# Kernel tuning notes

Measured on AMD Instinct MI355X. Metric: run time of the kernel, lower is better.

The kernel has to match this reference:

```python
import jax, jax.numpy as jnp
import numpy as np

EPS = 1e-8
LN_EPS = 1e-5
DIM, NHEADS = 512, 8
HEAD_DIM = DIM // NHEADS
SCALE = HEAD_DIM ** -0.5
ROLE_VOCAB = 8


def _layernorm(x, g, b):
    mu = x.mean(-1, keepdims=True)
    var = ((x - mu) ** 2).mean(-1, keepdims=True)
    return (x - mu) * jax.lax.rsqrt(var + LN_EPS) * g + b


def setup_inputs() -> dict:
    key = jax.random.key(0)
    ks = jax.random.split(key, 16)
    B, K, L, D = 8, 4, 1024, DIM
    s = 1.0 / np.sqrt(D)
    return {
        "state_repr": jax.random.normal(ks[0], (B, K, L, D), jnp.float32),
        "residue_mask": jax.random.randint(ks[1], (B, K, L), 0, 2) > 0,
        "state_weights": jax.random.uniform(ks[2], (B, K), jnp.float32),
        "state_roles": jax.random.randint(ks[3], (B, K), 0, ROLE_VOCAB),
        "state_present_mask": jnp.ones((B, K), dtype=bool),
        "role_emb": jax.random.normal(ks[4], (ROLE_VOCAB, D), jnp.float32),
        "Wq": jax.random.normal(ks[5], (D, D), jnp.float32) * s,
        "Wk": jax.random.normal(ks[6], (D, D), jnp.float32) * s,
        "Wv": jax.random.normal(ks[7], (D, D), jnp.float32) * s,
        "Wo": jax.random.normal(ks[8], (D, D), jnp.float32) * s,
        "ln1_g": jnp.ones((3 * D,), jnp.float32),
        "ln1_b": jnp.zeros((3 * D,), jnp.float32),
        "Wg1": jax.random.normal(ks[9], (D, 3 * D), jnp.float32) / np.sqrt(3 * D),
        "bg1": jnp.zeros((D,), jnp.float32),
        "Wg2": jax.random.normal(ks[10], (D, D), jnp.float32) * s,
        "bg2": jnp.zeros((D,), jnp.float32),
        "norm_g": jnp.ones((D,), jnp.float32),
        "norm_b": jnp.zeros((D,), jnp.float32),
    }


def _forward(state_repr, residue_mask, state_weights, state_roles, state_present_mask,
             role_emb, Wq, Wk, Wv, Wo, ln1_g, ln1_b, Wg1, bg1, Wg2, bg2, norm_g, norm_b):
    B, K, L, D = state_repr.shape
    H, hd = NHEADS, HEAD_DIM
    roles = jnp.maximum(state_roles, 0)
    role_e = role_emb[roles][:, :, None, :]                       # [B,K,1,D]
    valid = residue_mask & state_present_mask[:, :, None]          # [B,K,L]

    # normalized state weights
    pres = state_present_mask.astype(jnp.float32)
    w = state_weights.astype(jnp.float32) * pres
    denom = w.sum(1, keepdims=True)
    fallback = pres / jnp.maximum(pres.sum(1, keepdims=True), 1.0)
    nsw = jnp.where(denom > EPS, w / jnp.maximum(denom, EPS), fallback)  # [B,K]

    x = (state_repr + role_e) * valid[..., None]
    x = x.transpose(0, 2, 1, 3)                                    # [B,L,K,D]
    valid_rlk = valid.transpose(0, 2, 1)                           # [B,L,K]

    def proj(W):  # torch Linear: y = x @ W.T
        return (x @ W.T).reshape(B, L, K, H, hd).transpose(0, 1, 3, 2, 4)  # [B,L,H,K,hd]

    q, k, v = proj(Wq), proj(Wk), proj(Wv)
    logits = jnp.einsum('blhqd,blhkd->blhqk', q, k) * SCALE
    logits = logits + jnp.log(jnp.maximum(nsw, EPS))[:, None, None, None, :]
    key_mask = valid_rlk[:, :, None, None, :]                      # [B,L,1,1,K]
    logits = jnp.where(key_mask, logits, -jnp.inf)
    attn = jax.nn.softmax(logits, axis=-1)
    attn = jnp.nan_to_num(attn, nan=0.0, posinf=0.0, neginf=0.0)
    attn_out = jnp.einsum('blhqk,blhkd->blhqd', attn, v)
    attn_out = attn_out.transpose(0, 1, 3, 2, 4).reshape(B, L, K, D)
    attn_out = (attn_out @ Wo.T) * valid_rlk[..., None]

    swr = nsw[:, None, :] * valid_rlk.astype(jnp.float32)          # [B,L,K]
    swr = swr / jnp.maximum(swr.sum(-1, keepdims=True), EPS)
    weighted_mean = jnp.sum(x * swr[..., None], axis=2)            # [B,L,D]
    attn_pooled = jnp.sum(attn_out * swr[..., None], axis=2)

    max_in = jnp.where(valid_rlk[..., None], x, -1e9)
    max_feat = max_in.max(axis=2)
    has_any = valid_rlk.any(axis=2, keepdims=True)
    max_feat = jnp.where(has_any, max_feat, 0.0)

    fusion_base = 0.5 * (attn_pooled + weighted_mean)
    gate_in = jnp.concatenate([attn_pooled, weighted_mean, max_feat], axis=-1)
    h = _layernorm(gate_in, ln1_g, ln1_b)
    h = jax.nn.gelu(h @ Wg1.T + bg1, approximate=False)
    gate = jax.nn.sigmoid(h @ Wg2.T + bg2)
    fused = gate * fusion_base + (1.0 - gate) * max_feat
    fused = _layernorm(fused + weighted_mean, norm_g, norm_b)

    attn_mean = attn.mean(axis=(2, 3))                             # [B,L,K]
    return fused, attn_pooled, weighted_mean, max_feat, attn_mean, nsw


def reference(state_repr, residue_mask, state_weights, state_roles, state_present_mask,
              role_emb, Wq, Wk, Wv, Wo, ln1_g, ln1_b, Wg1, bg1, Wg2, bg2, norm_g, norm_b):
    return _forward(state_repr, residue_mask, state_weights, state_roles, state_present_mask,
                    role_emb, Wq, Wk, Wv, Wo, ln1_g, ln1_b, Wg1, bg1, Wg2, bg2, norm_g, norm_b)
```

## Files before the change

kernel.cpp:

```cpp
#include <hip/hip_runtime.h>
#include <math.h>

#define BB 8
#define KK 4
#define LL 1024
#define DD 512
#define HD 64
#define D3 1536
#define MM (BB*LL*KK)
#define BL (BB*LL)
#define SCALE 0.125f
#define EPSF 1e-8f
#define LN_EPSF 1e-5f

typedef _Float16 hfrag __attribute__((ext_vector_type(8)));
typedef float f32x4 __attribute__((ext_vector_type(4)));

__device__ __forceinline__ unsigned short f2h(float f) {
    _Float16 h = (_Float16)f;
    unsigned short u; __builtin_memcpy(&u, &h, 2); return u;
}
__device__ __forceinline__ float h2f(unsigned short u) {
    _Float16 h; __builtin_memcpy(&h, &u, 2); return (float)h;
}

__device__ __forceinline__ void glds16(const unsigned short* g, unsigned short* l) {
    __builtin_amdgcn_global_load_lds(
        (const __attribute__((address_space(1))) void*)g,
        (__attribute__((address_space(3))) void*)l, 16, 0, 0);
}

__device__ __forceinline__ void nsw_compute(const float* sw, const int* pres,
                                            int b, float* nswv) {
    float w[KK], pr[KK]; float denom = 0.f, ps = 0.f;
    #pragma unroll
    for (int k = 0; k < KK; ++k) {
        pr[k] = pres[b*KK + k] ? 1.f : 0.f;
        w[k]  = sw[b*KK + k] * pr[k];
        denom += w[k]; ps += pr[k];
    }
    #pragma unroll
    for (int k = 0; k < KK; ++k)
        nswv[k] = (denom > EPSF) ? w[k] / fmaxf(denom, EPSF)
                                 : pr[k] / fmaxf(ps, 1.f);
}

#define WSZ 262144
#define OG1 1048576
#define OG2 1835008
#define WTOT 2097152
__global__ __launch_bounds__(256) void cvt_weights(
        const float* __restrict__ Wq, const float* __restrict__ Wk,
        const float* __restrict__ Wv, const float* __restrict__ Wo,
        const float* __restrict__ Wg1, const float* __restrict__ Wg2,
        unsigned short* __restrict__ dst) {
    int t = blockIdx.x * 256 + threadIdx.x;
    int e = t * 4;
    const float* src; int off;
    if      (e < WSZ)    { src = Wq;  off = e; }
    else if (e < 2*WSZ)  { src = Wk;  off = e - WSZ; }
    else if (e < 3*WSZ)  { src = Wv;  off = e - 2*WSZ; }
    else if (e < OG1)    { src = Wo;  off = e - 3*WSZ; }
    else if (e < OG2)    { src = Wg1; off = e - OG1; }
    else                 { src = Wg2; off = e - OG2; }
    float4 v = *(const float4*)(src + off);
    ushort4 o;
    o.x = f2h(v.x); o.y = f2h(v.y); o.z = f2h(v.z); o.w = f2h(v.w);
    *(ushort4*)(dst + e) = o;
}

__global__ __launch_bounds__(256) void buildx_kernel(
        const float* __restrict__ SR, const int* __restrict__ residue,
        const int* __restrict__ pres, const int* __restrict__ roles,
        const float* __restrict__ role_emb, const float* __restrict__ sw,
        unsigned short* __restrict__ Xh, float* __restrict__ rowmask,
        float* __restrict__ out_wm, float* __restrict__ out_mx,
        float* __restrict__ f_nsw) {
    int t  = blockIdx.x * 256 + threadIdx.x;
    int bl = t >> 7;
    int d4 = (t & 127) << 2;
    int b  = bl >> 10, l = bl & 1023;
    float nswv[KK];
    nsw_compute(sw, pres, b, nswv);
    float mk[KK], swr[KK];
    float ssum = 0.f, many = 0.f;
    #pragma unroll
    for (int k = 0; k < KK; ++k) {
        int bk = b*KK + k;
        bool valid = (residue[(size_t)bk*LL + l] != 0) && (pres[bk] != 0);
        mk[k]  = valid ? 1.f : 0.f;
        swr[k] = nswv[k] * mk[k];
        ssum += swr[k]; many += mk[k];
    }
    float inv = 1.f / fmaxf(ssum, EPSF);
    bool hasany = many > 0.5f;
    float wmx = 0.f, wmy = 0.f, wmz = 0.f, wmw = 0.f;
    float mxx = -1e9f, mxy = -1e9f, mxz = -1e9f, mxw = -1e9f;
    #pragma unroll
    for (int k = 0; k < KK; ++k) {
        int bk = b*KK + k;
        int role = roles[bk]; if (role < 0) role = 0;
        float4 sr = *(const float4*)(SR + ((size_t)bk*LL + l)*DD + d4);
        float4 re = *(const float4*)(role_emb + (size_t)role*DD + d4);
        float xx = (sr.x + re.x)*mk[k], xy = (sr.y + re.y)*mk[k];
        float xz = (sr.z + re.z)*mk[k], xw = (sr.w + re.w)*mk[k];
        ushort4 xs; xs.x = f2h(xx); xs.y = f2h(xy); xs.z = f2h(xz); xs.w = f2h(xw);
        *(ushort4*)(Xh + (size_t)(bl*KK + k)*DD + d4) = xs;
        float s = swr[k]*inv;
        wmx = fmaf(xx, s, wmx); wmy = fmaf(xy, s, wmy);
        wmz = fmaf(xz, s, wmz); wmw = fmaf(xw, s, wmw);
        if (mk[k] > 0.5f) {
            mxx = fmaxf(mxx, xx); mxy = fmaxf(mxy, xy);
            mxz = fmaxf(mxz, xz); mxw = fmaxf(mxw, xw);
        }
    }
    if (!hasany) { mxx = mxy = mxz = mxw = 0.f; }
    float4 wmv; wmv.x = wmx; wmv.y = wmy; wmv.z = wmz; wmv.w = wmw;
    float4 mxv; mxv.x = mxx; mxv.y = mxy; mxv.z = mxz; mxv.w = mxw;
    *(float4*)(out_wm + (size_t)bl*DD + d4) = wmv;
    *(float4*)(out_mx + (size_t)bl*DD + d4) = mxv;
    if (d4 == 0) {
        #pragma unroll
        for (int k = 0; k < KK; ++k) rowmask[bl*KK + k] = mk[k];
    }
    if (blockIdx.x == 0 && threadIdx.x < BB*KK) {
        int bb = threadIdx.x >> 2, kk2 = threadIdx.x & 3;
        float nv[KK];
        nsw_compute(sw, pres, bb, nv);
        f_nsw[threadIdx.x] = nv[kk2];
    }
}

__global__ __launch_bounds__(512, 4) void gemm_qkv_8p(
        const unsigned short* __restrict__ A, const unsigned short* __restrict__ W,
        unsigned short* __restrict__ Cbase) {
    __shared__ __align__(16) unsigned short smem[36864];
    const int tid  = threadIdx.x;
    const int wave = tid >> 6, lane = tid & 63;
    const int id = blockIdx.x;
    const int wg = (id & 7) * 192 + (id >> 3);
    const int m0 = (wg / 12) * 256;
    const int n0 = (wg % 12) * 128;
    const int wm = wave >> 1, wn = wave & 1;
    const int fr = lane & 15, q = lane >> 4;
    const int srow = tid >> 2, scc = tid & 3;
    const int sswz = (scc ^ ((srow >> 1) & 3)) << 3;
    const unsigned short* Ag0 = A + (size_t)(m0 + srow)*512 + sswz;
    const unsigned short* Ag1 = Ag0 + (size_t)128*512;
    const unsigned short* Wg0 = W + (size_t)(n0 + srow)*512 + sswz;
    const int lA0 = tid << 3;
    const int lA1 = (tid + 512) << 3;
    int aoff[4], boff[4];
    #pragma unroll
    for (int mf = 0; mf < 4; ++mf) {
        int row = (wm << 6) + (mf << 4) + fr;
        aoff[mf] = (row << 5) + ((q ^ ((row >> 1) & 3)) << 3);
    }
    #pragma unroll
    for (int nf = 0; nf < 4; ++nf) {
        int row = (wn << 6) + (nf << 4) + fr;
        boff[nf] = (row << 5) + ((q ^ ((row >> 1) & 3)) << 3);
    }
    f32x4 acc[4][4] = {};

#define VMWAIT(N) asm volatile("s_waitcnt vmcnt(" #N ")" ::: "memory")
#define STAGE(tt) do { unsigned short* _d = smem + ((tt) % 3) * 12288; \
        const int _ko = (tt) << 5; \
        glds16(Ag0 + _ko, _d + lA0); glds16(Ag1 + _ko, _d + lA1); \
        glds16(Wg0 + _ko, _d + 8192 + lA0); } while (0)
#define MFROW(ai, areg) \
        acc[ai][0] = __builtin_amdgcn_mfma_f32_16x16x32_f16(areg, b0, acc[ai][0], 0, 0, 0); \
        acc[ai][1] = __builtin_amdgcn_mfma_f32_16x16x32_f16(areg, b1, acc[ai][1], 0, 0, 0); \
        acc[ai][2] = __builtin_amdgcn_mfma_f32_16x16x32_f16(areg, b2, acc[ai][2], 0, 0, 0); \
        acc[ai][3] = __builtin_amdgcn_mfma_f32_16x16x32_f16(areg, b3, acc[ai][3], 0, 0, 0);
#define TILE(t, STG, VM) do { \
        const unsigned short* _Ab = smem + ((t) % 3) * 12288; \
        const unsigned short* _Bb = _Ab + 8192; \
        VMWAIT(VM); \
        __builtin_amdgcn_s_barrier(); \
        __builtin_amdgcn_sched_barrier(0); \
        hfrag b0 = *(const hfrag*)(_Bb + boff[0]); \
        hfrag b1 = *(const hfrag*)(_Bb + boff[1]); \
        hfrag b2 = *(const hfrag*)(_Bb + boff[2]); \
        hfrag b3 = *(const hfrag*)(_Bb + boff[3]); \
        hfrag a0_ = *(const hfrag*)(_Ab + aoff[0]); \
        hfrag a1_ = *(const hfrag*)(_Ab + aoff[1]); \
        hfrag a2_ = *(const hfrag*)(_Ab + aoff[2]); \
        hfrag a3_ = *(const hfrag*)(_Ab + aoff[3]); \
        if (STG) STAGE((t) + 2); \
        __builtin_amdgcn_s_setprio(1); \
        MFROW(0, a0_) MFROW(1, a1_) MFROW(2, a2_) MFROW(3, a3_) \
        __builtin_amdgcn_s_setprio(0); \
    } while (0)

    STAGE(0); STAGE(1);
    #pragma unroll
    for (int t = 0; t < 14; ++t) TILE(t, 1, 3);
    TILE(14, 0, 3);
    TILE(15, 0, 0);
#undef TILE
#undef MFROW
#undef STAGE
#undef VMWAIT

    const int gc0 = n0 + (wn << 6);
    const int seg = gc0 >> 9;
    unsigned short* Cs = Cbase + (size_t)seg * ((size_t)MM * 512);
    const int cb = gc0 & 511;
    #pragma unroll
    for (int mf = 0; mf < 4; ++mf) {
        const int grow = m0 + (wm << 6) + (mf << 4) + (q << 2);
        #pragma unroll
        for (int nf = 0; nf < 4; ++nf) {
            const int col = cb + (nf << 4) + fr;
            #pragma unroll
            for (int r = 0; r < 4; ++r)
                Cs[(size_t)(grow + r) * 512 + col] = f2h(acc[mf][nf][r]);
        }
    }
}

__global__ __launch_bounds__(512, 4) void wo_gemm(
        const unsigned short* __restrict__ A,
        const unsigned short* __restrict__ W,
        const float* __restrict__ sw, const int* __restrict__ pres,
        const float* __restrict__ rmask, float* __restrict__ out_ap) {
    __shared__ __align__(16) unsigned short smem[36864];
    const int tid  = threadIdx.x;
    const int wave = tid >> 6, lane = tid & 63;
    const int id = blockIdx.x;
    const int wg = (id & 7) * 64 + (id >> 3);
    const int m0 = (wg >> 2) * 256;
    const int n0 = (wg & 3) * 128;
    const int wm = wave >> 1, wn = wave & 1;
    const int fr = lane & 15, q = lane >> 4;
    const int srow = tid >> 2, scc = tid & 3;
    const int sswz = (scc ^ ((srow >> 1) & 3)) << 3;
    const unsigned short* Ag0 = A + (size_t)(m0 + srow)*512 + sswz;
    const unsigned short* Ag1 = Ag0 + (size_t)128*512;
    const unsigned short* Wg0 = W + (size_t)(n0 + srow)*512 + sswz;
    const int lA0 = tid << 3;
    const int lA1 = (tid + 512) << 3;
    int aoff[4], boff[4];
    #pragma unroll
    for (int mf = 0; mf < 4; ++mf) {
        int row = (wm << 6) + (mf << 4) + fr;
        aoff[mf] = (row << 5) + ((q ^ ((row >> 1) & 3)) << 3);
    }
    #pragma unroll
    for (int nf = 0; nf < 4; ++nf) {
        int row = (wn << 6) + (nf << 4) + fr;
        boff[nf] = (row << 5) + ((q ^ ((row >> 1) & 3)) << 3);
    }
    f32x4 acc[4][4] = {};

#define VMWAIT(N) asm volatile("s_waitcnt vmcnt(" #N ")" ::: "memory")
#define STAGE(tt) do { unsigned short* _d = smem + ((tt) % 3) * 12288; \
        const int _ko = (tt) << 5; \
        glds16(Ag0 + _ko, _d + lA0); glds16(Ag1 + _ko, _d + lA1); \
        glds16(Wg0 + _ko, _d + 8192 + lA0); } while (0)
#define MFROW(ai, areg) \
        acc[ai][0] = __builtin_amdgcn_mfma_f32_16x16x32_f16(areg, b0, acc[ai][0], 0, 0, 0); \
        acc[ai][1] = __builtin_amdgcn_mfma_f32_16x16x32_f16(areg, b1, acc[ai][1], 0, 0, 0); \
        acc[ai][2] = __builtin_amdgcn_mfma_f32_16x16x32_f16(areg, b2, acc[ai][2], 0, 0, 0); \
        acc[ai][3] = __builtin_amdgcn_mfma_f32_16x16x32_f16(areg, b3, acc[ai][3], 0, 0, 0);
#define TILE(t, STG, VM) do { \
        const unsigned short* _Ab = smem + ((t) % 3) * 12288; \
        const unsigned short* _Bb = _Ab + 8192; \
        VMWAIT(VM); \
        __builtin_amdgcn_s_barrier(); \
        __builtin_amdgcn_sched_barrier(0); \
        hfrag b0 = *(const hfrag*)(_Bb + boff[0]); \
        hfrag b1 = *(const hfrag*)(_Bb + boff[1]); \
        hfrag b2 = *(const hfrag*)(_Bb + boff[2]); \
        hfrag b3 = *(const hfrag*)(_Bb + boff[3]); \
        hfrag a0_ = *(const hfrag*)(_Ab + aoff[0]); \
        hfrag a1_ = *(const hfrag*)(_Ab + aoff[1]); \
        hfrag a2_ = *(const hfrag*)(_Ab + aoff[2]); \
        hfrag a3_ = *(const hfrag*)(_Ab + aoff[3]); \
        if (STG) STAGE((t) + 2); \
        __builtin_amdgcn_s_setprio(1); \
        MFROW(0, a0_) MFROW(1, a1_) MFROW(2, a2_) MFROW(3, a3_) \
        __builtin_amdgcn_s_setprio(0); \
    } while (0)

    STAGE(0); STAGE(1);
    #pragma unroll
    for (int t = 0; t < 14; ++t) TILE(t, 1, 3);
    TILE(14, 0, 3);
    TILE(15, 0, 0);
#undef TILE
#undef MFROW
#undef STAGE
#undef VMWAIT

    const int b = (m0 >> 2) >> 10;
    float nv[KK];
    nsw_compute(sw, pres, b, nv);
    #pragma unroll
    for (int mf = 0; mf < 4; ++mf) {
        const int grow = m0 + (wm << 6) + (mf << 4) + (q << 2);
        const int bl = grow >> 2;
        float s4[KK]; float ssum = 0.f;
        #pragma unroll
        for (int k = 0; k < KK; ++k) { s4[k] = nv[k] * rmask[bl*4 + k]; ssum += s4[k]; }
        const float inv = 1.f / fmaxf(ssum, EPSF);
        #pragma unroll
        for (int nf = 0; nf < 4; ++nf) {
            const int col = n0 + (wn << 6) + (nf << 4) + fr;
            float ap = 0.f;
            #pragma unroll
            for (int r = 0; r < KK; ++r) ap = fmaf(s4[r]*inv, acc[mf][nf][r], ap);
            out_ap[(size_t)bl*512 + col] = ap;
        }
    }
}

__global__ __launch_bounds__(256) void ln1_kernel(
        const float* __restrict__ ap, const float* __restrict__ wm,
        const float* __restrict__ mx, const float* __restrict__ g,
        const float* __restrict__ bvec, unsigned short* __restrict__ hin) {
    const int bl = blockIdx.x * 4 + (threadIdx.x >> 6);
    const int lane = threadIdx.x & 63;
    const int c0 = lane * 8;
    float4 v[3][2];
    const float* srcs[3] = { ap + (size_t)bl*512 + c0,
                             wm + (size_t)bl*512 + c0,
                             mx + (size_t)bl*512 + c0 };
    float s = 0.f, s2 = 0.f;
    #pragma unroll
    for (int sg = 0; sg < 3; ++sg) {
        v[sg][0] = *(const float4*)(srcs[sg]);
        v[sg][1] = *(const float4*)(srcs[sg] + 4);
        #pragma unroll
        for (int e = 0; e < 8; ++e) {
            float x = ((const float*)v[sg])[e];
            s += x; s2 += x*x;
        }
    }
    #pragma unroll
    for (int o = 1; o < 64; o <<= 1) {
        s  += __shfl_xor(s,  o, 64);
        s2 += __shfl_xor(s2, o, 64);
    }
    const float mu = s * (1.f/(float)D3);
    const float var = s2 * (1.f/(float)D3) - mu*mu;
    const float rstd = rsqrtf(var + LN_EPSF);
    #pragma unroll
    for (int sg = 0; sg < 3; ++sg) {
        const int gofs = sg*512 + c0;
        #pragma unroll
        for (int h = 0; h < 2; ++h) {
            float4 g4 = *(const float4*)(g + gofs + h*4);
            float4 b4 = *(const float4*)(bvec + gofs + h*4);
            const float* sv = (const float*)&v[sg][h];
            ushort4 o4;
            o4.x = f2h((sv[0]-mu)*rstd*g4.x + b4.x);
            o4.y = f2h((sv[1]-mu)*rstd*g4.y + b4.y);
            o4.z = f2h((sv[2]-mu)*rstd*g4.z + b4.z);
            o4.w = f2h((sv[3]-mu)*rstd*g4.w + b4.w);
            *(ushort4*)(hin + (size_t)bl*D3 + gofs + h*4) = o4;
        }
    }
}

__global__ __launch_bounds__(256, 3) void gemm_g1(
        const unsigned short* __restrict__ A, const unsigned short* __restrict__ W,
        unsigned short* __restrict__ C, const float* __restrict__ bias) {
    __shared__ __align__(16) unsigned short smem[24576];
    const int tid  = threadIdx.x;
    const int wave = tid >> 6, lane = tid & 63;
    const int id = blockIdx.x;
    const int wg = (id & 7) * 32 + (id >> 3);
    const int m0 = (wg >> 2) * 128;
    const int n0 = (wg & 3) * 128;
    const int wm = wave >> 1, wn = wave & 1;
    const int fr = lane & 15, q = lane >> 4;
    const int srow = tid >> 2, scc = tid & 3;
    const int sswz = (scc ^ ((srow >> 1) & 3)) << 3;
    const unsigned short* Ag0 = A + (size_t)(m0 + srow)*D3 + sswz;
    const unsigned short* Ag1 = Ag0 + (size_t)64*D3;
    const unsigned short* Wg0 = W + (size_t)(n0 + srow)*D3 + sswz;
    const unsigned short* Wg1p = Wg0 + (size_t)64*D3;
    const int lA0 = tid << 3;
    const int lA1 = (tid + 256) << 3;
    int aoff[4], boff[4];
    #pragma unroll
    for (int mf = 0; mf < 4; ++mf) {
        int row = (wm << 6) + (mf << 4) + fr;
        aoff[mf] = (row << 5) + ((q ^ ((row >> 1) & 3)) << 3);
    }
    #pragma unroll
    for (int nf = 0; nf < 4; ++nf) {
        int row = (wn << 6) + (nf << 4) + fr;
        boff[nf] = (row << 5) + ((q ^ ((row >> 1) & 3)) << 3);
    }
    f32x4 acc[4][4] = {};

#define VMWAIT(N) asm volatile("s_waitcnt vmcnt(" #N ")" ::: "memory")
#define STAGE(tt) do { unsigned short* _d = smem + ((tt) % 3) * 8192; \
        const int _ko = (tt) << 5; \
        glds16(Ag0 + _ko, _d + lA0); glds16(Ag1 + _ko, _d + lA1); \
        glds16(Wg0 + _ko, _d + 4096 + lA0); glds16(Wg1p + _ko, _d + 4096 + lA1); } while (0)
#define MFROW(ai, areg) \
        acc[ai][0] = __builtin_amdgcn_mfma_f32_16x16x32_f16(areg, b0, acc[ai][0], 0, 0, 0); \
        acc[ai][1] = __builtin_amdgcn_mfma_f32_16x16x32_f16(areg, b1, acc[ai][1], 0, 0, 0); \
        acc[ai][2] = __builtin_amdgcn_mfma_f32_16x16x32_f16(areg, b2, acc[ai][2], 0, 0, 0); \
        acc[ai][3] = __builtin_amdgcn_mfma_f32_16x16x32_f16(areg, b3, acc[ai][3], 0, 0, 0);
#define TILE(t, STG, VM) do { \
        const unsigned short* _Ab = smem + ((t) % 3) * 8192; \
        const unsigned short* _Bb = _Ab + 4096; \
        VMWAIT(VM); \
        __builtin_amdgcn_s_barrier(); \
        __builtin_amdgcn_sched_barrier(0); \
        hfrag b0 = *(const hfrag*)(_Bb + boff[0]); \
        hfrag b1 = *(const hfrag*)(_Bb + boff[1]); \
        hfrag b2 = *(const hfrag*)(_Bb + boff[2]); \
        hfrag b3 = *(const hfrag*)(_Bb + boff[3]); \
        hfrag a0_ = *(const hfrag*)(_Ab + aoff[0]); \
        hfrag a1_ = *(const hfrag*)(_Ab + aoff[1]); \
        hfrag a2_ = *(const hfrag*)(_Ab + aoff[2]); \
        hfrag a3_ = *(const hfrag*)(_Ab + aoff[3]); \
        if (STG) STAGE((t) + 2); \
        __builtin_amdgcn_s_setprio(1); \
        MFROW(0, a0_) MFROW(1, a1_) MFROW(2, a2_) MFROW(3, a3_) \
        __builtin_amdgcn_s_setprio(0); \
    } while (0)

    STAGE(0); STAGE(1);
    #pragma unroll 3
    for (int t = 0; t < 46; ++t) TILE(t, 1, 4);
    TILE(46, 0, 4);
    TILE(47, 0, 0);
#undef TILE
#undef MFROW
#undef STAGE
#undef VMWAIT

    #pragma unroll
    for (int mf = 0; mf < 4; ++mf) {
        const int grow = m0 + (wm << 6) + (mf << 4) + (q << 2);
        #pragma unroll
        for (int nf = 0; nf < 4; ++nf) {
            const int col = n0 + (wn << 6) + (nf << 4) + fr;
            const float bv = bias[col];
            #pragma unroll
            for (int r = 0; r < 4; ++r) {
                float v = acc[mf][nf][r] + bv;
                v = 0.5f * v * (1.f + erff(v * 0.70710678118654752f));
                C[(size_t)(grow + r) * 512 + col] = f2h(v);
            }
        }
    }
}

__global__ __launch_bounds__(256, 3) void wg2_gemm(
        const unsigned short* __restrict__ A,
        const unsigned short* __restrict__ W,
        const float* __restrict__ bg2,
        const float* __restrict__ in_ap, const float* __restrict__ in_wm,
        const float* __restrict__ in_mx, float* __restrict__ pre) {
    __shared__ __align__(16) unsigned short smem[24576];
    const int tid  = threadIdx.x;
    const int wave = tid >> 6, lane = tid & 63;
    const int id = blockIdx.x;
    const int wg = (id & 7) * 32 + (id >> 3);
    const int m0 = (wg >> 2) * 128;
    const int n0 = (wg & 3) * 128;
    const int wm = wave >> 1, wn = wave & 1;
    const int fr = lane & 15, q = lane >> 4;
    const int srow = tid >> 2, scc = tid & 3;
    const int sswz = (scc ^ ((srow >> 1) & 3)) << 3;
    const unsigned short* Ag0 = A + (size_t)(m0 + srow)*512 + sswz;
    const unsigned short* Ag1 = Ag0 + (size_t)64*512;
    const unsigned short* Wg0 = W + (size_t)(n0 + srow)*512 + sswz;
    const unsigned short* Wg1p = Wg0 + (size_t)64*512;
    const int lA0 = tid << 3;
    const int lA1 = (tid + 256) << 3;
    int aoff[4], boff[4];
    #pragma unroll
    for (int mf = 0; mf < 4; ++mf) {
        int row = (wm << 6) + (mf << 4) + fr;
        aoff[mf] = (row << 5) + ((q ^ ((row >> 1) & 3)) << 3);
    }
    #pragma unroll
    for (int nf = 0; nf < 4; ++nf) {
        int row = (wn << 6) + (nf << 4) + fr;
        boff[nf] = (row << 5) + ((q ^ ((row >> 1) & 3)) << 3);
    }
    f32x4 acc[4][4] = {};

#define VMWAIT(N) asm volatile("s_waitcnt vmcnt(" #N ")" ::: "memory")
#define STAGE(tt) do { unsigned short* _d = smem + ((tt) % 3) * 8192; \
        const int _ko = (tt) << 5; \
        glds16(Ag0 + _ko, _d + lA0); glds16(Ag1 + _ko, _d + lA1); \
        glds16(Wg0 + _ko, _d + 4096 + lA0); glds16(Wg1p + _ko, _d + 4096 + lA1); } while (0)
#define MFROW(ai, areg) \
        acc[ai][0] = __builtin_amdgcn_mfma_f32_16x16x32_f16(areg, b0, acc[ai][0], 0, 0, 0); \
        acc[ai][1] = __builtin_amdgcn_mfma_f32_16x16x32_f16(areg, b1, acc[ai][1], 0, 0, 0); \
        acc[ai][2] = __builtin_amdgcn_mfma_f32_16x16x32_f16(areg, b2, acc[ai][2], 0, 0, 0); \
        acc[ai][3] = __builtin_amdgcn_mfma_f32_16x16x32_f16(areg, b3, acc[ai][3], 0, 0, 0);
#define TILE(t, STG, VM) do { \
        const unsigned short* _Ab = smem + ((t) % 3) * 8192; \
        const unsigned short* _Bb = _Ab + 4096; \
        VMWAIT(VM); \
        __builtin_amdgcn_s_barrier(); \
        __builtin_amdgcn_sched_barrier(0); \
        hfrag b0 = *(const hfrag*)(_Bb + boff[0]); \
        hfrag b1 = *(const hfrag*)(_Bb + boff[1]); \
        hfrag b2 = *(const hfrag*)(_Bb + boff[2]); \
        hfrag b3 = *(const hfrag*)(_Bb + boff[3]); \
        hfrag a0_ = *(const hfrag*)(_Ab + aoff[0]); \
        hfrag a1_ = *(const hfrag*)(_Ab + aoff[1]); \
        hfrag a2_ = *(const hfrag*)(_Ab + aoff[2]); \
        hfrag a3_ = *(const hfrag*)(_Ab + aoff[3]); \
        if (STG) STAGE((t) + 2); \
        __builtin_amdgcn_s_setprio(1); \
        MFROW(0, a0_) MFROW(1, a1_) MFROW(2, a2_) MFROW(3, a3_) \
        __builtin_amdgcn_s_setprio(0); \
    } while (0)

    STAGE(0); STAGE(1);
    #pragma unroll
    for (int t = 0; t < 14; ++t) TILE(t, 1, 4);
    TILE(14, 0, 4);
    TILE(15, 0, 0);
#undef TILE
#undef MFROW
#undef STAGE
#undef VMWAIT

    #pragma unroll
    for (int mf = 0; mf < 4; ++mf) {
        const int grow = m0 + (wm << 6) + (mf << 4) + (q << 2);
        #pragma unroll
        for (int nf = 0; nf < 4; ++nf) {
            const int col = n0 + (wn << 6) + (nf << 4) + fr;
            const float bv = bg2[col];
            #pragma unroll
            for (int r = 0; r < 4; ++r) {
                const int row = grow + r;
                float g = 1.f / (1.f + expf(-(acc[mf][nf][r] + bv)));
                float ap = in_ap[(size_t)row*512 + col];
                float wmv = in_wm[(size_t)row*512 + col];
                float mxv = in_mx[(size_t)row*512 + col];
                pre[(size_t)row*512 + col] = g*0.5f*(ap + wmv) + (1.f - g)*mxv + wmv;
            }
        }
    }
}

__global__ __launch_bounds__(256) void final_ln_kernel(
        const float* __restrict__ pre, const float* __restrict__ ng,
        const float* __restrict__ nb, float* __restrict__ fused) {
    const int row = blockIdx.x * 4 + (threadIdx.x >> 6);
    const int lane = threadIdx.x & 63;
    const int c0 = lane * 8;
    float4 p0 = *(const float4*)(pre + (size_t)row*512 + c0);
    float4 p1 = *(const float4*)(pre + (size_t)row*512 + c0 + 4);
    float s = 0.f, s2 = 0.f;
    const float* pv = (const float*)&p0;
    #pragma unroll
    for (int e = 0; e < 4; ++e) { s += pv[e]; s2 += pv[e]*pv[e]; }
    pv = (const float*)&p1;
    #pragma unroll
    for (int e = 0; e < 4; ++e) { s += pv[e]; s2 += pv[e]*pv[e]; }
    #pragma unroll
    for (int o = 1; o < 64; o <<= 1) {
        s  += __shfl_xor(s,  o, 64);
        s2 += __shfl_xor(s2, o, 64);
    }
    const float mu = s * (1.f/(float)DD);
    const float var = s2 * (1.f/(float)DD) - mu*mu;
    const float rstd = rsqrtf(var + LN_EPSF);
    float4 g0 = *(const float4*)(ng + c0), g1 = *(const float4*)(ng + c0 + 4);
    float4 b0 = *(const float4*)(nb + c0), b1 = *(const float4*)(nb + c0 + 4);
    float4 o0, o1;
    o0.x = (p0.x-mu)*rstd*g0.x + b0.x; o0.y = (p0.y-mu)*rstd*g0.y + b0.y;
    o0.z = (p0.z-mu)*rstd*g0.z + b0.z; o0.w = (p0.w-mu)*rstd*g0.w + b0.w;
    o1.x = (p1.x-mu)*rstd*g1.x + b1.x; o1.y = (p1.y-mu)*rstd*g1.y + b1.y;
    o1.z = (p1.z-mu)*rstd*g1.z + b1.z; o1.w = (p1.w-mu)*rstd*g1.w + b1.w;
    *(float4*)(fused + (size_t)row*512 + c0) = o0;
    *(float4*)(fused + (size_t)row*512 + c0 + 4) = o1;
}

__global__ __launch_bounds__(256) void attn_kernel(
        unsigned short* Qb ,
        const unsigned short* __restrict__ Kb, const unsigned short* __restrict__ Vb,
        const float* __restrict__ sw, const int* __restrict__ pres,
        const float* __restrict__ rowmask,
        float* __restrict__ attn_mean_out) {
    __shared__ float att[128];
    __shared__ float lw[KK], mk[KK];
    int bl = blockIdx.x, b = bl >> 10, mb = bl * KK;
    int tid = threadIdx.x;
    if (tid < KK) {
        float nv[KK];
        nsw_compute(sw, pres, b, nv);
        lw[tid] = logf(fmaxf(nv[tid], EPSF));
        mk[tid] = rowmask[mb + tid];
    }
    __syncthreads();
    if (tid < 128) {
        int h = tid >> 4, i = (tid >> 2) & 3, j = tid & 3;
        const unsigned short* qp = Qb + (size_t)(mb + i)*DD + h*HD;
        const unsigned short* kp = Kb + (size_t)(mb + j)*DD + h*HD;
        float s = 0.f;
        #pragma unroll
        for (int c = 0; c < 8; ++c) {
            hfrag qv = *(const hfrag*)(qp + c*8);
            hfrag kv = *(const hfrag*)(kp + c*8);
            #pragma unroll
            for (int e = 0; e < 8; ++e)
                s = fmaf((float)qv[e], (float)kv[e], s);
        }
        float lg = s * SCALE + lw[j];
        att[tid] = (mk[j] > 0.5f) ? lg : -INFINITY;
    }
    __syncthreads();
    if (tid < 32) {
        int base = tid * 4;
        float l0 = att[base], l1 = att[base+1], l2 = att[base+2], l3 = att[base+3];
        float m = fmaxf(fmaxf(l0, l1), fmaxf(l2, l3));
        if (m == -INFINITY) {
            att[base] = att[base+1] = att[base+2] = att[base+3] = 0.f;
        } else {
            float e0 = expf(l0 - m), e1 = expf(l1 - m), e2 = expf(l2 - m), e3 = expf(l3 - m);
            float inv = 1.f / (e0 + e1 + e2 + e3);
            att[base] = e0*inv; att[base+1] = e1*inv; att[base+2] = e2*inv; att[base+3] = e3*inv;
        }
    }
    __syncthreads();
    if (tid < KK) {
        float s = 0.f;
        for (int hi = 0; hi < 32; ++hi) s += att[hi*4 + tid];
        attn_mean_out[(size_t)bl*KK + tid] = s * (1.f/32.f);
    }
    #pragma unroll
    for (int p = 0; p < 4; ++p) {
        int idx = p*256 + tid;
        int i = idx >> 8, d2 = (idx & 255) << 1, h = d2 >> 6;
        float s0 = 0.f, s1 = 0.f;
        #pragma unroll
        for (int j = 0; j < KK; ++j) {
            float aj = att[h*16 + i*4 + j];
            ushort2 vv = *(const ushort2*)(Vb + (size_t)(mb + j)*DD + d2);
            s0 = fmaf(aj, h2f(vv.x), s0);
            s1 = fmaf(aj, h2f(vv.y), s1);
        }
        ushort2 o; o.x = f2h(s0); o.y = f2h(s1);
        *(ushort2*)(Qb + (size_t)(mb + i)*DD + d2) = o;
    }
}

extern "C" void kernel_launch(void* const* d_in, const int* in_sizes, int n_in,
                              void* d_out, int out_size, void* d_ws, size_t ws_size,
                              hipStream_t stream) {
    const float* SR      = (const float*)d_in[0];
    const int*   residue = (const int*)d_in[1];
    const float* sw      = (const float*)d_in[2];
    const int*   roles   = (const int*)d_in[3];
    const int*   pres    = (const int*)d_in[4];
    const float* role_emb= (const float*)d_in[5];
    const float* Wq      = (const float*)d_in[6];
    const float* Wk      = (const float*)d_in[7];
    const float* Wv      = (const float*)d_in[8];
    const float* Wo      = (const float*)d_in[9];
    const float* ln1_g   = (const float*)d_in[10];
    const float* ln1_b   = (const float*)d_in[11];
    const float* Wg1     = (const float*)d_in[12];
    const float* bg1     = (const float*)d_in[13];
    const float* Wg2     = (const float*)d_in[14];
    const float* bg2     = (const float*)d_in[15];
    const float* norm_g  = (const float*)d_in[16];
    const float* norm_b  = (const float*)d_in[17];

    float* out = (float*)d_out;
    const size_t BLD = (size_t)BL * DD;
    float* f_fused = out;
    float* f_ap    = out + BLD;
    float* f_wm    = out + 2*BLD;
    float* f_mx    = out + 3*BLD;
    float* f_am    = out + 4*BLD;
    float* f_nsw   = out + 4*BLD + (size_t)BL*KK;

    char* base = (char*)d_ws;
    const size_t MD2 = (size_t)MM * DD * 2;
    unsigned short* Xh = (unsigned short*)(base);
    unsigned short* Qh = (unsigned short*)(base + MD2);
    unsigned short* Kh = (unsigned short*)(base + 2*MD2);
    unsigned short* Vh = (unsigned short*)(base + 3*MD2);
    unsigned short* Wb = (unsigned short*)(base + 4*MD2);
    float* rmask = (float*)(base + 4*MD2 + (size_t)WTOT*2);
    unsigned short* AOh  = Qh;
    unsigned short* Hin  = Vh;
    unsigned short* Hbuf = Xh;
    float* preb = (float*)Kh;
    const unsigned short* Wqkv = Wb;
    const unsigned short* Woh  = Wb + 3*WSZ;
    const unsigned short* Wg1h = Wb + OG1;
    const unsigned short* Wg2h = Wb + OG2;

    dim3 blk(256);

    cvt_weights<<<WTOT/1024, blk, 0, stream>>>(Wq, Wk, Wv, Wo, Wg1, Wg2, Wb);
    buildx_kernel<<<(BL*128)/256, blk, 0, stream>>>(SR, residue, pres, roles, role_emb,
                                                    sw, Xh, rmask, f_wm, f_mx, f_nsw);

    gemm_qkv_8p<<<dim3(1536), dim3(512), 0, stream>>>(Xh, Wqkv, Qh);

    attn_kernel<<<BL, blk, 0, stream>>>(Qh, Kh, Vh, sw, pres, rmask, f_am);

    wo_gemm<<<dim3(512), dim3(512), 0, stream>>>(
        AOh, Woh, sw, pres, rmask, f_ap);

    ln1_kernel<<<dim3(BL/4), blk, 0, stream>>>(
        f_ap, f_wm, f_mx, ln1_g, ln1_b, Hin);

    gemm_g1<<<dim3(256), blk, 0, stream>>>(Hin, Wg1h, Hbuf, bg1);

    wg2_gemm<<<dim3(256), blk, 0, stream>>>(
        Hbuf, Wg2h, bg2, f_ap, f_wm, f_mx, preb);

    final_ln_kernel<<<dim3(BL/4), blk, 0, stream>>>(
        preb, norm_g, norm_b, f_fused);
}
```

Before: 335.2 us.

## Pool attention outputs over states before Wo projection to shrink GEMM

Because the state-weighted pooling over K is linear, the attention kernel now folds the pooling weights into the attention probabilities and writes one pooled value vector per residue. The output projection then runs on a BL×512 matrix instead of a (BL·K)×512 one, so the Wo GEMM does a quarter of the work and no longer has to write the per-state attention output. The attention kernel also writes less data. The cost is a small extra reduction inside the attention kernel and a slightly different rounding order because fp16 rounding now happens after pooling rather than before.

```diff
diff --git a/kernel.cpp b/kernel.cpp
--- a/kernel.cpp
+++ b/kernel.cpp
@@ -220,153 +220,89 @@
     }
 }
 
-__global__ __launch_bounds__(512, 4) void wo_gemm(
+__global__ __launch_bounds__(256) void attn_kernel(
+        const unsigned short* __restrict__ Qb, const unsigned short* __restrict__ Kb,
+        const unsigned short* __restrict__ Vb,
+        unsigned short* __restrict__ pooled,
+        const float* __restrict__ sw, const int* __restrict__ pres,
+        const float* __restrict__ rowmask,
+        float* __restrict__ attn_mean_out) {
+    __shared__ float att[128];
+    __shared__ float wv[32];
+    __shared__ float lw[KK], mk[KK], sp[KK];
+    int bl = blockIdx.x, b = bl >> 10, mb = bl * KK;
+    int tid = threadIdx.x;
+    if (tid < KK) {
+        float nv[KK];
+        nsw_compute(sw, pres, b, nv);
+        lw[tid] = logf(fmaxf(nv[tid], EPSF));
+        float mkk[KK]; float ssum = 0.f;
+        #pragma unroll
+        for (int k = 0; k < KK; ++k) { mkk[k] = rowmask[mb + k]; ssum += nv[k]*mkk[k]; }
+        mk[tid] = mkk[tid];
+        sp[tid] = nv[tid]*mkk[tid] / fmaxf(ssum, EPSF);
+    }
+    __syncthreads();
+    if (tid < 128) {
+        int h = tid >> 4, i = (tid >> 2) & 3, j = tid & 3;
+        const unsigned short* qp = Qb + (size_t)(mb + i)*DD + h*HD;
+        const unsigned short* kp = Kb + (size_t)(mb + j)*DD + h*HD;
+        float s = 0.f;
+        #pragma unroll
+        for (int c = 0; c < 8; ++c) {
+            hfrag qv = *(const hfrag*)(qp + c*8);
+            hfrag kv = *(const hfrag*)(kp + c*8);
+            #pragma unroll
+            for (int e = 0; e < 8; ++e)
+                s = fmaf((float)qv[e], (float)kv[e], s);
+        }
+        float lg = s * SCALE + lw[j];
+        att[tid] = (mk[j] > 0.5f) ? lg : -INFINITY;
+    }
+    __syncthreads();
+    if (tid < 32) {
+        int base = tid * 4;
+        float l0 = att[base], l1 = att[base+1], l2 = att[base+2], l3 = att[base+3];
+        float m = fmaxf(fmaxf(l0, l1), fmaxf(l2, l3));
+        if (m == -INFINITY) {
+            att[base] = att[base+1] = att[base+2] = att[base+3] = 0.f;
+        } else {
+            float e0 = expf(l0 - m), e1 = expf(l1 - m), e2 = expf(l2 - m), e3 = expf(l3 - m);
+            float inv = 1.f / (e0 + e1 + e2 + e3);
+            att[base] = e0*inv; att[base+1] = e1*inv; att[base+2] = e2*inv; att[base+3] = e3*inv;
+        }
+    }
+    __syncthreads();
+    if (tid < KK) {
+        float s = 0.f;
+        for (int hi = 0; hi < 32; ++hi) s += att[hi*4 + tid];
+        attn_mean_out[(size_t)bl*KK + tid] = s * (1.f/32.f);
+    }
+    if (tid < 32) {
+        int h = tid >> 2, j = tid & 3;
+        wv[tid] = sp[0]*att[h*16 + 0*4 + j] + sp[1]*att[h*16 + 1*4 + j]
+                + sp[2]*att[h*16 + 2*4 + j] + sp[3]*att[h*16 + 3*4 + j];
+    }
+    __syncthreads();
+    {
+        int d2 = tid << 1, h = d2 >> 6;
+        float s0 = 0.f, s1 = 0.f;
+        #pragma unroll
+        for (int j = 0; j < KK; ++j) {
+            float aj = wv[h*4 + j];
+            ushort2 vvv = *(const ushort2*)(Vb + (size_t)(mb + j)*DD + d2);
+            s0 = fmaf(aj, h2f(vvv.x), s0);
+            s1 = fmaf(aj, h2f(vvv.y), s1);
+        }
+        ushort2 o; o.x = f2h(s0); o.y = f2h(s1);
+        *(ushort2*)(pooled + (size_t)bl*DD + d2) = o;
+    }
+}
+
+__global__ __launch_bounds__(256, 3) void ap_gemm(
         const unsigned short* __restrict__ A,
         const unsigned short* __restrict__ W,
-        const float* __restrict__ sw, const int* __restrict__ pres,
-        const float* __restrict__ rmask, float* __restrict__ out_ap) {
-    __shared__ __align__(16) unsigned short smem[36864];
-    const int tid  = threadIdx.x;
-    const int wave = tid >> 6, lane = tid & 63;
-    const int id = blockIdx.x;
-    const int wg = (id & 7) * 64 + (id >> 3);
-    const int m0 = (wg >> 2) * 256;
-    const int n0 = (wg & 3) * 128;
-    const int wm = wave >> 1, wn = wave & 1;
-    const int fr = lane & 15, q = lane >> 4;
-    const int srow = tid >> 2, scc = tid & 3;
-    const int sswz = (scc ^ ((srow >> 1) & 3)) << 3;
-    const unsigned short* Ag0 = A + (size_t)(m0 + srow)*512 + sswz;
-    const unsigned short* Ag1 = Ag0 + (size_t)128*512;
-    const unsigned short* Wg0 = W + (size_t)(n0 + srow)*512 + sswz;
-    const int lA0 = tid << 3;
-    const int lA1 = (tid + 512) << 3;
-    int aoff[4], boff[4];
-    #pragma unroll
-    for (int mf = 0; mf < 4; ++mf) {
-        int row = (wm << 6) + (mf << 4) + fr;
-        aoff[mf] = (row << 5) + ((q ^ ((row >> 1) & 3)) << 3);
-    }
-    #pragma unroll
-    for (int nf = 0; nf < 4; ++nf) {
-        int row = (wn << 6) + (nf << 4) + fr;
-        boff[nf] = (row << 5) + ((q ^ ((row >> 1) & 3)) << 3);
-    }
-    f32x4 acc[4][4] = {};
-
-#define VMWAIT(N) asm volatile("s_waitcnt vmcnt(" #N ")" ::: "memory")
-#define STAGE(tt) do { unsigned short* _d = smem + ((tt) % 3) * 12288; \
-        const int _ko = (tt) << 5; \
-        glds16(Ag0 + _ko, _d + lA0); glds16(Ag1 + _ko, _d + lA1); \
-        glds16(Wg0 + _ko, _d + 8192 + lA0); } while (0)
-#define MFROW(ai, areg) \
-        acc[ai][0] = __builtin_amdgcn_mfma_f32_16x16x32_f16(areg, b0, acc[ai][0], 0, 0, 0); \
-        acc[ai][1] = __builtin_amdgcn_mfma_f32_16x16x32_f16(areg, b1, acc[ai][1], 0, 0, 0); \
-        acc[ai][2] = __builtin_amdgcn_mfma_f32_16x16x32_f16(areg, b2, acc[ai][2], 0, 0, 0); \
-        acc[ai][3] = __builtin_amdgcn_mfma_f32_16x16x32_f16(areg, b3, acc[ai][3], 0, 0, 0);
-#define TILE(t, STG, VM) do { \
-        const unsigned short* _Ab = smem + ((t) % 3) * 12288; \
-        const unsigned short* _Bb = _Ab + 8192; \
-        VMWAIT(VM); \
-        __builtin_amdgcn_s_barrier(); \
-        __builtin_amdgcn_sched_barrier(0); \
-        hfrag b0 = *(const hfrag*)(_Bb + boff[0]); \
-        hfrag b1 = *(const hfrag*)(_Bb + boff[1]); \
-        hfrag b2 = *(const hfrag*)(_Bb + boff[2]); \
-        hfrag b3 = *(const hfrag*)(_Bb + boff[3]); \
-        hfrag a0_ = *(const hfrag*)(_Ab + aoff[0]); \
-        hfrag a1_ = *(const hfrag*)(_Ab + aoff[1]); \
-        hfrag a2_ = *(const hfrag*)(_Ab + aoff[2]); \
-        hfrag a3_ = *(const hfrag*)(_Ab + aoff[3]); \
-        if (STG) STAGE((t) + 2); \
-        __builtin_amdgcn_s_setprio(1); \
-        MFROW(0, a0_) MFROW(1, a1_) MFROW(2, a2_) MFROW(3, a3_) \
-        __builtin_amdgcn_s_setprio(0); \
-    } while (0)
-
-    STAGE(0); STAGE(1);
-    #pragma unroll
-    for (int t = 0; t < 14; ++t) TILE(t, 1, 3);
-    TILE(14, 0, 3);
-    TILE(15, 0, 0);
-#undef TILE
-#undef MFROW
-#undef STAGE
-#undef VMWAIT
-
-    const int b = (m0 >> 2) >> 10;
-    float nv[KK];
-    nsw_compute(sw, pres, b, nv);
-    #pragma unroll
-    for (int mf = 0; mf < 4; ++mf) {
-        const int grow = m0 + (wm << 6) + (mf << 4) + (q << 2);
-        const int bl = grow >> 2;
-        float s4[KK]; float ssum = 0.f;
-        #pragma unroll
-        for (int k = 0; k < KK; ++k) { s4[k] = nv[k] * rmask[bl*4 + k]; ssum += s4[k]; }
-        const float inv = 1.f / fmaxf(ssum, EPSF);
-        #pragma unroll
-        for (int nf = 0; nf < 4; ++nf) {
-            const int col = n0 + (wn << 6) + (nf << 4) + fr;
-            float ap = 0.f;
-            #pragma unroll
-            for (int r = 0; r < KK; ++r) ap = fmaf(s4[r]*inv, acc[mf][nf][r], ap);
-            out_ap[(size_t)bl*512 + col] = ap;
-        }
-    }
-}
-
-__global__ __launch_bounds__(256) void ln1_kernel(
-        const float* __restrict__ ap, const float* __restrict__ wm,
-        const float* __restrict__ mx, const float* __restrict__ g,
-        const float* __restrict__ bvec, unsigned short* __restrict__ hin) {
-    const int bl = blockIdx.x * 4 + (threadIdx.x >> 6);
-    const int lane = threadIdx.x & 63;
-    const int c0 = lane * 8;
-    float4 v[3][2];
-    const float* srcs[3] = { ap + (size_t)bl*512 + c0,
-                             wm + (size_t)bl*512 + c0,
-                             mx + (size_t)bl*512 + c0 };
-    float s = 0.f, s2 = 0.f;
-    #pragma unroll
-    for (int sg = 0; sg < 3; ++sg) {
-        v[sg][0] = *(const float4*)(srcs[sg]);
-        v[sg][1] = *(const float4*)(srcs[sg] + 4);
-        #pragma unroll
-        for (int e = 0; e < 8; ++e) {
-            float x = ((const float*)v[sg])[e];
-            s += x; s2 += x*x;
-        }
-    }
-    #pragma unroll
-    for (int o = 1; o < 64; o <<= 1) {
-        s  += __shfl_xor(s,  o, 64);
-        s2 += __shfl_xor(s2, o, 64);
-    }
-    const float mu = s * (1.f/(float)D3);
-    const float var = s2 * (1.f/(float)D3) - mu*mu;
-    const float rstd = rsqrtf(var + LN_EPSF);
-    #pragma unroll
-    for (int sg = 0; sg < 3; ++sg) {
-        const int gofs = sg*512 + c0;
-        #pragma unroll
-        for (int h = 0; h < 2; ++h) {
-            float4 g4 = *(const float4*)(g + gofs + h*4);
-            float4 b4 = *(const float4*)(bvec + gofs + h*4);
-            const float* sv = (const float*)&v[sg][h];
-            ushort4 o4;
-            o4.x = f2h((sv[0]-mu)*rstd*g4.x + b4.x);
-            o4.y = f2h((sv[1]-mu)*rstd*g4.y + b4.y);
-            o4.z = f2h((sv[2]-mu)*rstd*g4.z + b4.z);
-            o4.w = f2h((sv[3]-mu)*rstd*g4.w + b4.w);
-            *(ushort4*)(hin + (size_t)bl*D3 + gofs + h*4) = o4;
-        }
-    }
-}
-
-__global__ __launch_bounds__(256, 3) void gemm_g1(
-        const unsigned short* __restrict__ A, const unsigned short* __restrict__ W,
-        unsigned short* __restrict__ C, const float* __restrict__ bias) {
+        float* __restrict__ out_ap) {
     __shared__ __align__(16) unsigned short smem[24576];
     const int tid  = threadIdx.x;
     const int wave = tid >> 6, lane = tid & 63;
@@ -378,10 +314,10 @@
     const int fr = lane & 15, q = lane >> 4;
     const int srow = tid >> 2, scc = tid & 3;
     const int sswz = (scc ^ ((srow >> 1) & 3)) << 3;
-    const unsigned short* Ag0 = A + (size_t)(m0 + srow)*D3 + sswz;
-    const unsigned short* Ag1 = Ag0 + (size_t)64*D3;
-    const unsigned short* Wg0 = W + (size_t)(n0 + srow)*D3 + sswz;
-    const unsigned short* Wg1p = Wg0 + (size_t)64*D3;
+    const unsigned short* Ag0 = A + (size_t)(m0 + srow)*512 + sswz;
+    const unsigned short* Ag1 = Ag0 + (size_t)64*512;
+    const unsigned short* Wg0 = W + (size_t)(n0 + srow)*512 + sswz;
+    const unsigned short* Wg1p = Wg0 + (size_t)64*512;
     const int lA0 = tid << 3;
     const int lA1 = (tid + 256) << 3;
     int aoff[4], boff[4];
@@ -428,10 +364,10 @@
     } while (0)
 
     STAGE(0); STAGE(1);
-    #pragma unroll 3
-    for (int t = 0; t < 46; ++t) TILE(t, 1, 4);
-    TILE(46, 0, 4);
-    TILE(47, 0, 0);
+    #pragma unroll
+    for (int t = 0; t < 14; ++t) TILE(t, 1, 4);
+    TILE(14, 0, 4);
+    TILE(15, 0, 0);
 #undef TILE
 #undef MFROW
 #undef STAGE
@@ -443,23 +379,64 @@
         #pragma unroll
         for (int nf = 0; nf < 4; ++nf) {
             const int col = n0 + (wn << 6) + (nf << 4) + fr;
-            const float bv = bias[col];
             #pragma unroll
-            for (int r = 0; r < 4; ++r) {
-                float v = acc[mf][nf][r] + bv;
-                v = 0.5f * v * (1.f + erff(v * 0.70710678118654752f));
-                C[(size_t)(grow + r) * 512 + col] = f2h(v);
-            }
-        }
-    }
-}
-
-__global__ __launch_bounds__(256, 3) void wg2_gemm(
-        const unsigned short* __restrict__ A,
-        const unsigned short* __restrict__ W,
-        const float* __restrict__ bg2,
-        const float* __restrict__ in_ap, const float* __restrict__ in_wm,
-        const float* __restrict__ in_mx, float* __restrict__ pre) {
+            for (int r = 0; r < 4; ++r)
+                out_ap[(size_t)(grow + r)*512 + col] = acc[mf][nf][r];
+        }
+    }
+}
+
+__global__ __launch_bounds__(256) void ln1_kernel(
+        const float* __restrict__ ap, const float* __restrict__ wm,
+        const float* __restrict__ mx, const float* __restrict__ g,
+        const float* __restrict__ bvec, unsigned short* __restrict__ hin) {
+    const int bl = blockIdx.x * 4 + (threadIdx.x >> 6);
+    const int lane = threadIdx.x & 63;
+    const int c0 = lane * 8;
+    float4 v[3][2];
+    const float* srcs[3] = { ap + (size_t)bl*512 + c0,
+                             wm + (size_t)bl*512 + c0,
+                             mx + (size_t)bl*512 + c0 };
+    float s = 0.f, s2 = 0.f;
+    #pragma unroll
+    for (int sg = 0; sg < 3; ++sg) {
+        v[sg][0] = *(const float4*)(srcs[sg]);
+        v[sg][1] = *(const float4*)(srcs[sg] + 4);
+        #pragma unroll
+        for (int e = 0; e < 8; ++e) {
+            float x = ((const float*)v[sg])[e];
+            s += x; s2 += x*x;
+        }
+    }
+    #pragma unroll
+    for (int o = 1; o < 64; o <<= 1) {
+        s  += __shfl_xor(s,  o, 64);
+        s2 += __shfl_xor(s2, o, 64);
+    }
+    const float mu = s * (1.f/(float)D3);
+    const float var = s2 * (1.f/(float)D3) - mu*mu;
+    const float rstd = rsqrtf(var + LN_EPSF);
+    #pragma unroll
+    for (int sg = 0; sg < 3; ++sg) {
+        const int gofs = sg*512 + c0;
+        #pragma unroll
+        for (int h = 0; h < 2; ++h) {
+            float4 g4 = *(const float4*)(g + gofs + h*4);
+            float4 b4 = *(const float4*)(bvec + gofs + h*4);
+            const float* sv = (const float*)&v[sg][h];
+            ushort4 o4;
+            o4.x = f2h((sv[0]-mu)*rstd*g4.x + b4.x);
+            o4.y = f2h((sv[1]-mu)*rstd*g4.y + b4.y);
+            o4.z = f2h((sv[2]-mu)*rstd*g4.z + b4.z);
+            o4.w = f2h((sv[3]-mu)*rstd*g4.w + b4.w);
+            *(ushort4*)(hin + (size_t)bl*D3 + gofs + h*4) = o4;
+        }
+    }
+}
+
+__global__ __launch_bounds__(256, 3) void gemm_g1(
+        const unsigned short* __restrict__ A, const unsigned short* __restrict__ W,
+        unsigned short* __restrict__ C, const float* __restrict__ bias) {
     __shared__ __align__(16) unsigned short smem[24576];
     const int tid  = threadIdx.x;
     const int wave = tid >> 6, lane = tid & 63;
@@ -471,10 +448,10 @@
     const int fr = lane & 15, q = lane >> 4;
     const int srow = tid >> 2, scc = tid & 3;
     const int sswz = (scc ^ ((srow >> 1) & 3)) << 3;
-    const unsigned short* Ag0 = A + (size_t)(m0 + srow)*512 + sswz;
-    const unsigned short* Ag1 = Ag0 + (size_t)64*512;
-    const unsigned short* Wg0 = W + (size_t)(n0 + srow)*512 + sswz;
-    const unsigned short* Wg1p = Wg0 + (size_t)64*512;
+    const unsigned short* Ag0 = A + (size_t)(m0 + srow)*D3 + sswz;
+    const unsigned short* Ag1 = Ag0 + (size_t)64*D3;
+    const unsigned short* Wg0 = W + (size_t)(n0 + srow)*D3 + sswz;
+    const unsigned short* Wg1p = Wg0 + (size_t)64*D3;
     const int lA0 = tid << 3;
     const int lA1 = (tid + 256) << 3;
     int aoff[4], boff[4];
@@ -521,6 +498,99 @@
     } while (0)
 
     STAGE(0); STAGE(1);
+    #pragma unroll 3
+    for (int t = 0; t < 46; ++t) TILE(t, 1, 4);
+    TILE(46, 0, 4);
+    TILE(47, 0, 0);
+#undef TILE
+#undef MFROW
+#undef STAGE
+#undef VMWAIT
+
+    #pragma unroll
+    for (int mf = 0; mf < 4; ++mf) {
+        const int grow = m0 + (wm << 6) + (mf << 4) + (q << 2);
+        #pragma unroll
+        for (int nf = 0; nf < 4; ++nf) {
+            const int col = n0 + (wn << 6) + (nf << 4) + fr;
+            const float bv = bias[col];
+            #pragma unroll
+            for (int r = 0; r < 4; ++r) {
+                float v = acc[mf][nf][r] + bv;
+                v = 0.5f * v * (1.f + erff(v * 0.70710678118654752f));
+                C[(size_t)(grow + r) * 512 + col] = f2h(v);
+            }
+        }
+    }
+}
+
+__global__ __launch_bounds__(256, 3) void wg2_gemm(
+        const unsigned short* __restrict__ A,
+        const unsigned short* __restrict__ W,
+        const float* __restrict__ bg2,
+        const float* __restrict__ in_ap, const float* __restrict__ in_wm,
+        const float* __restrict__ in_mx, float* __restrict__ pre) {
+    __shared__ __align__(16) unsigned short smem[24576];
+    const int tid  = threadIdx.x;
+    const int wave = tid >> 6, lane = tid & 63;
+    const int id = blockIdx.x;
+    const int wg = (id & 7) * 32 + (id >> 3);
+    const int m0 = (wg >> 2) * 128;
+    const int n0 = (wg & 3) * 128;
+    const int wm = wave >> 1, wn = wave & 1;
+    const int fr = lane & 15, q = lane >> 4;
+    const int srow = tid >> 2, scc = tid & 3;
+    const int sswz = (scc ^ ((srow >> 1) & 3)) << 3;
+    const unsigned short* Ag0 = A + (size_t)(m0 + srow)*512 + sswz;
+    const unsigned short* Ag1 = Ag0 + (size_t)64*512;
+    const unsigned short* Wg0 = W + (size_t)(n0 + srow)*512 + sswz;
+    const unsigned short* Wg1p = Wg0 + (size_t)64*512;
+    const int lA0 = tid << 3;
+    const int lA1 = (tid + 256) << 3;
+    int aoff[4], boff[4];
+    #pragma unroll
+    for (int mf = 0; mf < 4; ++mf) {
+        int row = (wm << 6) + (mf << 4) + fr;
+        aoff[mf] = (row << 5) + ((q ^ ((row >> 1) & 3)) << 3);
+    }
+    #pragma unroll
+    for (int nf = 0; nf < 4; ++nf) {
+        int row = (wn << 6) + (nf << 4) + fr;
+        boff[nf] = (row << 5) + ((q ^ ((row >> 1) & 3)) << 3);
+    }
+    f32x4 acc[4][4] = {};
+
+#define VMWAIT(N) asm volatile("s_waitcnt vmcnt(" #N ")" ::: "memory")
+#define STAGE(tt) do { unsigned short* _d = smem + ((tt) % 3) * 8192; \
+        const int _ko = (tt) << 5; \
+        glds16(Ag0 + _ko, _d + lA0); glds16(Ag1 + _ko, _d + lA1); \
+        glds16(Wg0 + _ko, _d + 4096 + lA0); glds16(Wg1p + _ko, _d + 4096 + lA1); } while (0)
+#define MFROW(ai, areg) \
+        acc[ai][0] = __builtin_amdgcn_mfma_f32_16x16x32_f16(areg, b0, acc[ai][0], 0, 0, 0); \
+        acc[ai][1] = __builtin_amdgcn_mfma_f32_16x16x32_f16(areg, b1, acc[ai][1], 0, 0, 0); \
+        acc[ai][2] = __builtin_amdgcn_mfma_f32_16x16x32_f16(areg, b2, acc[ai][2], 0, 0, 0); \
+        acc[ai][3] = __builtin_amdgcn_mfma_f32_16x16x32_f16(areg, b3, acc[ai][3], 0, 0, 0);
+#define TILE(t, STG, VM) do { \
+        const unsigned short* _Ab = smem + ((t) % 3) * 8192; \
+        const unsigned short* _Bb = _Ab + 4096; \
+        VMWAIT(VM); \
+        __builtin_amdgcn_s_barrier(); \
+        __builtin_amdgcn_sched_barrier(0); \
+        hfrag b0 = *(const hfrag*)(_Bb + boff[0]); \
+        hfrag b1 = *(const hfrag*)(_Bb + boff[1]); \
+        hfrag b2 = *(const hfrag*)(_Bb + boff[2]); \
+        hfrag b3 = *(const hfrag*)(_Bb + boff[3]); \
+        hfrag a0_ = *(const hfrag*)(_Ab + aoff[0]); \
+        hfrag a1_ = *(const hfrag*)(_Ab + aoff[1]); \
+        hfrag a2_ = *(const hfrag*)(_Ab + aoff[2]); \
+        hfrag a3_ = *(const hfrag*)(_Ab + aoff[3]); \
+        if (STG) STAGE((t) + 2); \
+        __builtin_amdgcn_s_setprio(1); \
+        MFROW(0, a0_) MFROW(1, a1_) MFROW(2, a2_) MFROW(3, a3_) \
+        __builtin_amdgcn_s_setprio(0); \
+    } while (0)
+
+    STAGE(0); STAGE(1);
     #pragma unroll
     for (int t = 0; t < 14; ++t) TILE(t, 1, 4);
     TILE(14, 0, 4);
@@ -582,75 +652,6 @@
     o1.z = (p1.z-mu)*rstd*g1.z + b1.z; o1.w = (p1.w-mu)*rstd*g1.w + b1.w;
     *(float4*)(fused + (size_t)row*512 + c0) = o0;
     *(float4*)(fused + (size_t)row*512 + c0 + 4) = o1;
-}
-
-__global__ __launch_bounds__(256) void attn_kernel(
-        unsigned short* Qb ,
-        const unsigned short* __restrict__ Kb, const unsigned short* __restrict__ Vb,
-        const float* __restrict__ sw, const int* __restrict__ pres,
-        const float* __restrict__ rowmask,
-        float* __restrict__ attn_mean_out) {
-    __shared__ float att[128];
-    __shared__ float lw[KK], mk[KK];
-    int bl = blockIdx.x, b = bl >> 10, mb = bl * KK;
-    int tid = threadIdx.x;
-    if (tid < KK) {
-        float nv[KK];
-        nsw_compute(sw, pres, b, nv);
-        lw[tid] = logf(fmaxf(nv[tid], EPSF));
-        mk[tid] = rowmask[mb + tid];
-    }
-    __syncthreads();
-    if (tid < 128) {
-        int h = tid >> 4, i = (tid >> 2) & 3, j = tid & 3;
-        const unsigned short* qp = Qb + (size_t)(mb + i)*DD + h*HD;
-        const unsigned short* kp = Kb + (size_t)(mb + j)*DD + h*HD;
-        float s = 0.f;
-        #pragma unroll
-        for (int c = 0; c < 8; ++c) {
-            hfrag qv = *(const hfrag*)(qp + c*8);
-            hfrag kv = *(const hfrag*)(kp + c*8);
-            #pragma unroll
-            for (int e = 0; e < 8; ++e)
-                s = fmaf((float)qv[e], (float)kv[e], s);
-        }
-        float lg = s * SCALE + lw[j];
-        att[tid] = (mk[j] > 0.5f) ? lg : -INFINITY;
-    }
-    __syncthreads();
-    if (tid < 32) {
-        int base = tid * 4;
-        float l0 = att[base], l1 = att[base+1], l2 = att[base+2], l3 = att[base+3];
-        float m = fmaxf(fmaxf(l0, l1), fmaxf(l2, l3));
-        if (m == -INFINITY) {
-            att[base] = att[base+1] = att[base+2] = att[base+3] = 0.f;
-        } else {
-            float e0 = expf(l0 - m), e1 = expf(l1 - m), e2 = expf(l2 - m), e3 = expf(l3 - m);
-            float inv = 1.f / (e0 + e1 + e2 + e3);
-            att[base] = e0*inv; att[base+1] = e1*inv; att[base+2] = e2*inv; att[base+3] = e3*inv;
-        }
-    }
-    __syncthreads();
-    if (tid < KK) {
-        float s = 0.f;
-        for (int hi = 0; hi < 32; ++hi) s += att[hi*4 + tid];
-        attn_mean_out[(size_t)bl*KK + tid] = s * (1.f/32.f);
-    }
-    #pragma unroll
-    for (int p = 0; p < 4; ++p) {
-        int idx = p*256 + tid;
-        int i = idx >> 8, d2 = (idx & 255) << 1, h = d2 >> 6;
-        float s0 = 0.f, s1 = 0.f;
-        #pragma unroll
-        for (int j = 0; j < KK; ++j) {
-            float aj = att[h*16 + i*4 + j];
-            ushort2 vv = *(const ushort2*)(Vb + (size_t)(mb + j)*DD + d2);
-            s0 = fmaf(aj, h2f(vv.x), s0);
-            s1 = fmaf(aj, h2f(vv.y), s1);
-        }
-        ushort2 o; o.x = f2h(s0); o.y = f2h(s1);
-        *(ushort2*)(Qb + (size_t)(mb + i)*DD + d2) = o;
-    }
 }
 
 extern "C" void kernel_launch(void* const* d_in, const int* in_sizes, int n_in,
@@ -692,7 +693,7 @@
     unsigned short* Vh = (unsigned short*)(base + 3*MD2);
     unsigned short* Wb = (unsigned short*)(base + 4*MD2);
     float* rmask = (float*)(base + 4*MD2 + (size_t)WTOT*2);
-    unsigned short* AOh  = Qh;
+    unsigned short* PVh  = Xh;
     unsigned short* Hin  = Vh;
     unsigned short* Hbuf = Xh;
     float* preb = (float*)Kh;
@@ -709,10 +710,9 @@
 
     gemm_qkv_8p<<<dim3(1536), dim3(512), 0, stream>>>(Xh, Wqkv, Qh);
 
-    attn_kernel<<<BL, blk, 0, stream>>>(Qh, Kh, Vh, sw, pres, rmask, f_am);
-
-    wo_gemm<<<dim3(512), dim3(512), 0, stream>>>(
-        AOh, Woh, sw, pres, rmask, f_ap);
+    attn_kernel<<<BL, blk, 0, stream>>>(Qh, Kh, Vh, PVh, sw, pres, rmask, f_am);
+
+    ap_gemm<<<dim3(256), blk, 0, stream>>>(PVh, Woh, f_ap);
 
     ln1_kernel<<<dim3(BL/4), blk, 0, stream>>>(
         f_ap, f_wm, f_mx, ln1_g, ln1_b, Hin);
```

Measured after the change: 314.3 us. -6.2%, faster.
